# Optimization experiments

Hardware: AMD Instinct MI355X
Metric: run time of the kernel (lower is better)

## Reference

```python
import jax, jax.numpy as jnp
import numpy as np

T = 10.0           # distillation temperature (init arg T)
LOSS_WEIGHT = 1.0  # module-level loss_weight (init arg)
EPS_STD = 1e-07
EPS_RATIO = 1e-08

ROWS, BINS = 1048576, 17  # (4*N, n+1), n = 16


def setup_inputs() -> dict:
    key = jax.random.key(0)
    k1, k2, k3 = jax.random.split(key, 3)
    pred = jax.random.normal(k1, (ROWS, BINS), dtype=jnp.float32)
    soft_label = jax.random.normal(k2, (ROWS, BINS), dtype=jnp.float32)
    weight = jax.random.uniform(k3, (ROWS,), dtype=jnp.float32)
    return {"pred": pred, "soft_label": soft_label, "weight": weight}


def _normalize(logit):
    # torch .std() is unbiased (ddof=1)
    mean = jnp.mean(logit, axis=-1, keepdims=True)
    stdv = jnp.std(logit, axis=-1, keepdims=True, ddof=1)
    return (logit - mean) / (EPS_STD + stdv)


def reference(pred, soft_label, weight):
    soft = jax.lax.stop_gradient(soft_label)  # detach_target=True

    # kd_loss_ls with logit_stand=True
    ls = _normalize(pred)
    lt = _normalize(soft)
    log_p_student = jax.nn.log_softmax(ls / T, axis=1)
    log_p_teacher = jax.nn.log_softmax(lt / T, axis=1)
    p_teacher = jnp.exp(log_p_teacher)
    # F.kl_div(log_pred, target, 'none') = target * (log(target) - log_pred)
    loss_ls = jnp.mean(jnp.sum(p_teacher * (log_p_teacher - log_p_student), axis=1)) * (T * T)

    # sum_distributions_loop on target = softmax(soft_label) -- batched full conv1d
    target = jax.nn.softmax(soft, axis=1)            # (4N, bins)
    n_rows, bins = target.shape
    N = n_rows // 4
    t = target.reshape(N, 4, bins)
    top, bottom, left, right = t[:, 0], t[:, 1], t[:, 2], t[:, 3]
    # pad+flip+conv1d in torch == true full convolution, length 2*bins-1 = 2n+1
    conv_full = jax.vmap(lambda a, b: jnp.convolve(a, b, mode='full'))
    sum_lr = conv_full(left, right)                   # (N, 2n+1)
    sum_tb = conv_full(top, bottom)                   # (N, 2n+1)
    target_ratio = sum_lr / (sum_tb + EPS_RATIO)

    # weighted_loss wrapper: loss * weight, then 'mean' reduction; outer * loss_weight
    loss = LOSS_WEIGHT * jnp.mean(loss_ls * weight)
    return loss, target_ratio
```

## Files before the change

### kernel.cpp

```cpp
#include <hip/hip_runtime.h>

#define ROWS 1048576
#define BINS 17
#define RPB 64
#define NBLK (ROWS / RPB)
#define GPB (RPB / 4)
#define CONV_N 33

template <bool PART>
__global__ __launch_bounds__(64, 4) void kd_main(
    const float* __restrict__ pred,
    const float* __restrict__ soft,
    const float* __restrict__ weight,
    float* __restrict__ out,
    float* __restrict__ ws)
{
    __shared__ float sA[RPB * BINS];
    __shared__ float sB[RPB * BINS];
    const int tid = threadIdx.x;
    const long long base = (long long)blockIdx.x * (RPB * BINS);

    const float4* p4 = reinterpret_cast<const float4*>(pred + base);
    const float4* q4 = reinterpret_cast<const float4*>(soft + base);
    float4* a4 = reinterpret_cast<float4*>(sA);
    float4* b4 = reinterpret_cast<float4*>(sB);
#pragma unroll
    for (int k = 0; k < 4; ++k) {
        a4[k * 64 + tid] = p4[k * 64 + tid];
        b4[k * 64 + tid] = q4[k * 64 + tid];
    }
    if (tid < 16) {
        a4[256 + tid] = p4[256 + tid];
        b4[256 + tid] = q4[256 + tid];
    }
    const float w = weight[blockIdx.x * RPB + tid];
    __syncthreads();

    float x[BINS], y[BINS];
    float sx = 0.f, sy = 0.f, xmx = -1e30f, ymx = -1e30f;
#pragma unroll
    for (int j = 0; j < BINS; ++j) {
        x[j] = sA[tid * BINS + j];
        y[j] = sB[tid * BINS + j];
        sx += x[j]; sy += y[j];
        xmx = fmaxf(xmx, x[j]); ymx = fmaxf(ymx, y[j]);
    }
    const float mx = sx * (1.0f / BINS);
    const float my = sy * (1.0f / BINS);

    float vx = 0.f, vy = 0.f;
#pragma unroll
    for (int j = 0; j < BINS; ++j) {
        const float dx = x[j] - mx; vx = fmaf(dx, dx, vx);
        const float dy = y[j] - my; vy = fmaf(dy, dy, vy);
    }
    const float invsx = 0.1f / (1e-7f + sqrtf(vx * (1.0f / (BINS - 1))));
    const float invsy = 0.1f / (1e-7f + sqrtf(vy * (1.0f / (BINS - 1))));
    const float amax = (xmx - mx) * invsx;
    const float bmax = (ymx - my) * invsy;

    float sea = 0.f, seb = 0.f, ts = 0.f;
#pragma unroll
    for (int j = 0; j < BINS; ++j) {
        sea += __expf((x[j] - mx) * invsx - amax);
        seb += __expf((y[j] - my) * invsy - bmax);
        ts  += __expf(y[j] - ymx);
    }
    const float la = __logf(sea);
    const float lb = __logf(seb);
    const float invseb = 1.0f / seb;
    const float invts  = 1.0f / ts;

    float kl = 0.f;
#pragma unroll
    for (int j = 0; j < BINS; ++j) {
        const float aj = (x[j] - mx) * invsx - amax;
        const float bj = (y[j] - my) * invsy - bmax;
        kl = fmaf(__expf(bj), (bj - lb) - (aj - la), kl);
    }
    kl *= invseb;

#pragma unroll
    for (int j = 0; j < BINS; ++j)
        sA[tid * BINS + j] = __expf(y[j] - ymx) * invts;

    float k2 = kl, w2 = w;
#pragma unroll
    for (int off = 32; off >= 1; off >>= 1) {
        k2 += __shfl_down(k2, off, 64);
        w2 += __shfl_down(w2, off, 64);
    }

    __syncthreads();

    float* sR = sB;

    if (tid < 2 * GPB) {
        const int g = tid >> 1;
        const int R = 4 * g + ((tid & 1) ? 0 : 2);
        float f[2 * BINS];
        const float2* pr = reinterpret_cast<const float2*>(&sA[R * BINS]);
#pragma unroll
        for (int i = 0; i < BINS; ++i) {
            const float2 v = pr[i];
            f[2 * i] = v.x; f[2 * i + 1] = v.y;
        }
        float accv[CONV_N];
#pragma unroll
        for (int j = 0; j < CONV_N; ++j) accv[j] = 0.f;
#pragma unroll
        for (int k = 0; k < BINS; ++k)
#pragma unroll
            for (int m = 0; m < BINS; ++m)
                accv[k + m] = fmaf(f[k], f[BINS + m], accv[k + m]);

#pragma unroll
        for (int j = 0; j < CONV_N; ++j) {
            const float o = __shfl_down(accv[j], 1, 64);
            if ((tid & 1) == 0)
                sR[g * CONV_N + j] = accv[j] / (o + 1e-8f);
        }
    }
    __syncthreads();

    const long long ob = 1 + (long long)blockIdx.x * (GPB * CONV_N);
#pragma unroll
    for (int i = 0; i < 8; ++i)
        out[ob + i * 64 + tid] = sR[i * 64 + tid];
    if (tid < 16) out[ob + 512 + tid] = sR[512 + tid];

    if (tid == 0) {
        if (PART) {
            ws[blockIdx.x]        = k2;
            ws[NBLK + blockIdx.x] = w2;
        } else {
            atomicAdd(&ws[0], k2);
            atomicAdd(&ws[1], w2);
        }
    }
}

template <bool PART>
__global__ __launch_bounds__(1024) void kd_reduce(
    const float* __restrict__ ws, float* __restrict__ out)
{
    if (!PART) {
        if (threadIdx.x == 0)
            out[0] = 100.0f * (ws[0] * (1.0f / ROWS)) * (ws[1] * (1.0f / ROWS));
        return;
    }
    __shared__ float red[32];
    const int tid = threadIdx.x;
    const float4* k4 = reinterpret_cast<const float4*>(ws);
    const float4* w4 = reinterpret_cast<const float4*>(ws + NBLK);
    float ks = 0.f, wsum = 0.f;
#pragma unroll
    for (int i = 0; i < 4; ++i) {
        const float4 a = k4[i * 1024 + tid];
        const float4 b = w4[i * 1024 + tid];
        ks += (a.x + a.y) + (a.z + a.w);
        wsum += (b.x + b.y) + (b.z + b.w);
    }
#pragma unroll
    for (int off = 32; off >= 1; off >>= 1) {
        ks += __shfl_down(ks, off, 64);
        wsum += __shfl_down(wsum, off, 64);
    }
    if ((tid & 63) == 0) {
        red[(tid >> 6) * 2 + 0] = ks;
        red[(tid >> 6) * 2 + 1] = wsum;
    }
    __syncthreads();
    if (tid == 0) {
        float K = 0.f, W = 0.f;
#pragma unroll
        for (int i = 0; i < 16; ++i) { K += red[2 * i]; W += red[2 * i + 1]; }
        out[0] = 100.0f * (K * (1.0f / ROWS)) * (W * (1.0f / ROWS));
    }
}

extern "C" void kernel_launch(void* const* d_in, const int* in_sizes, int n_in,
                              void* d_out, int out_size, void* d_ws, size_t ws_size,
                              hipStream_t stream)
{
    const float* pred   = (const float*)d_in[0];
    const float* soft   = (const float*)d_in[1];
    const float* weight = (const float*)d_in[2];
    float* out = (float*)d_out;
    float* ws  = (float*)d_ws;

    if (ws_size >= (size_t)(2 * NBLK) * sizeof(float)) {
        kd_main<true><<<NBLK, RPB, 0, stream>>>(pred, soft, weight, out, ws);
        kd_reduce<true><<<1, 1024, 0, stream>>>(ws, out);
    } else {
        hipMemsetAsync(ws, 0, 2 * sizeof(float), stream);
        kd_main<false><<<NBLK, RPB, 0, stream>>>(pred, soft, weight, out, ws);
        kd_reduce<false><<<1, 1024, 0, stream>>>(ws, out);
    }
}
```

Baseline: 183.3 us.

## Double rows per block and fuse softmax/KL math into one exp2 pass

Raises rows per block from 64 to 128, writing two per-wave partials per block, and rewrites the per-row statistics as a single pass. Variance now comes from sum and sum of squares, the log-softmax terms are folded into exp2 with a precomputed scale, and the KL is computed from one accumulated sum instead of a second exp loop. Divisions use hardware reciprocal approximations. Risks include reduced precision from the single-pass variance, and only half the block's threads doing the convolution stage.

Result: no change. 183.0 us (-0.2%).

```diff
diff --git a/kernel.cpp b/kernel.cpp
--- a/kernel.cpp
+++ b/kernel.cpp
@@ -2,13 +2,16 @@
 
 #define ROWS 1048576
 #define BINS 17
-#define RPB 64
+#define RPB 128
 #define NBLK (ROWS / RPB)
+#define NPART (2 * NBLK)
 #define GPB (RPB / 4)
 #define CONV_N 33
+#define L2E 1.442695040888963f
+#define LN2 0.6931471805599453f
 
 template <bool PART>
-__global__ __launch_bounds__(64, 4) void kd_main(
+__global__ __launch_bounds__(128, 4) void kd_main(
     const float* __restrict__ pred,
     const float* __restrict__ soft,
     const float* __restrict__ weight,
@@ -26,63 +29,58 @@
     float4* b4 = reinterpret_cast<float4*>(sB);
 #pragma unroll
     for (int k = 0; k < 4; ++k) {
-        a4[k * 64 + tid] = p4[k * 64 + tid];
-        b4[k * 64 + tid] = q4[k * 64 + tid];
+        a4[k * RPB + tid] = p4[k * RPB + tid];
+        b4[k * RPB + tid] = q4[k * RPB + tid];
     }
-    if (tid < 16) {
-        a4[256 + tid] = p4[256 + tid];
-        b4[256 + tid] = q4[256 + tid];
+    if (tid < 32) {
+        a4[512 + tid] = p4[512 + tid];
+        b4[512 + tid] = q4[512 + tid];
     }
     const float w = weight[blockIdx.x * RPB + tid];
     __syncthreads();
 
     float x[BINS], y[BINS];
-    float sx = 0.f, sy = 0.f, xmx = -1e30f, ymx = -1e30f;
+    float sx = 0.f, sy = 0.f, sxx = 0.f, syy = 0.f;
+    float xmx = -1e30f, ymx = -1e30f;
 #pragma unroll
     for (int j = 0; j < BINS; ++j) {
         x[j] = sA[tid * BINS + j];
         y[j] = sB[tid * BINS + j];
-        sx += x[j]; sy += y[j];
-        xmx = fmaxf(xmx, x[j]); ymx = fmaxf(ymx, y[j]);
+        sx += x[j]; sxx = fmaf(x[j], x[j], sxx); xmx = fmaxf(xmx, x[j]);
+        sy += y[j]; syy = fmaf(y[j], y[j], syy); ymx = fmaxf(ymx, y[j]);
     }
     const float mx = sx * (1.0f / BINS);
     const float my = sy * (1.0f / BINS);
+    const float vx = fmaxf(fmaf(-sx, mx, sxx), 0.f) * (1.0f / (BINS - 1));
+    const float vy = fmaxf(fmaf(-sy, my, syy), 0.f) * (1.0f / (BINS - 1));
+    const float sxl = (0.1f * L2E) *
+        __builtin_amdgcn_rcpf(1e-7f + __builtin_amdgcn_sqrtf(vx));
+    const float syl = (0.1f * L2E) *
+        __builtin_amdgcn_rcpf(1e-7f + __builtin_amdgcn_sqrtf(vy));
+    const float cA = -xmx * sxl;
+    const float cB = -ymx * syl;
+    const float cT = -ymx * L2E;
 
-    float vx = 0.f, vy = 0.f;
+    float et[BINS];
+    float sea = 0.f, seb = 0.f, ts = 0.f, sdb = 0.f;
 #pragma unroll
     for (int j = 0; j < BINS; ++j) {
-        const float dx = x[j] - mx; vx = fmaf(dx, dx, vx);
-        const float dy = y[j] - my; vy = fmaf(dy, dy, vy);
+        const float aj = fmaf(x[j], sxl, cA);
+        const float bj = fmaf(y[j], syl, cB);
+        const float ea = exp2f(aj);
+        const float eb = exp2f(bj);
+        const float tv = exp2f(fmaf(y[j], L2E, cT));
+        sea += ea; seb += eb; ts += tv;
+        sdb = fmaf(eb, bj - aj, sdb);
+        et[j] = tv;
     }
-    const float invsx = 0.1f / (1e-7f + sqrtf(vx * (1.0f / (BINS - 1))));
-    const float invsy = 0.1f / (1e-7f + sqrtf(vy * (1.0f / (BINS - 1))));
-    const float amax = (xmx - mx) * invsx;
-    const float bmax = (ymx - my) * invsy;
-
-    float sea = 0.f, seb = 0.f, ts = 0.f;
-#pragma unroll
-    for (int j = 0; j < BINS; ++j) {
-        sea += __expf((x[j] - mx) * invsx - amax);
-        seb += __expf((y[j] - my) * invsy - bmax);
-        ts  += __expf(y[j] - ymx);
-    }
-    const float la = __logf(sea);
-    const float lb = __logf(seb);
-    const float invseb = 1.0f / seb;
-    const float invts  = 1.0f / ts;
-
-    float kl = 0.f;
-#pragma unroll
-    for (int j = 0; j < BINS; ++j) {
-        const float aj = (x[j] - mx) * invsx - amax;
-        const float bj = (y[j] - my) * invsy - bmax;
-        kl = fmaf(__expf(bj), (bj - lb) - (aj - la), kl);
-    }
-    kl *= invseb;
+    const float kl = LN2 * (sdb * __builtin_amdgcn_rcpf(seb)
+                            + (__log2f(sea) - __log2f(seb)));
+    const float invts = __builtin_amdgcn_rcpf(ts);
 
 #pragma unroll
     for (int j = 0; j < BINS; ++j)
-        sA[tid * BINS + j] = __expf(y[j] - ymx) * invts;
+        sA[tid * BINS + j] = et[j] * invts;
 
     float k2 = kl, w2 = w;
 #pragma unroll
@@ -90,12 +88,22 @@
         k2 += __shfl_down(k2, off, 64);
         w2 += __shfl_down(w2, off, 64);
     }
+    if ((tid & 63) == 0) {
+        const int wv = tid >> 6;
+        if (PART) {
+            ws[2 * blockIdx.x + wv]         = k2;
+            ws[NPART + 2 * blockIdx.x + wv] = w2;
+        } else {
+            atomicAdd(&ws[0], k2);
+            atomicAdd(&ws[1], w2);
+        }
+    }
 
     __syncthreads();
 
     float* sR = sB;
 
-    if (tid < 2 * GPB) {
+    if (tid < 64) {
         const int g = tid >> 1;
         const int R = 4 * g + ((tid & 1) ? 0 : 2);
         float f[2 * BINS];
@@ -118,7 +126,8 @@
         for (int j = 0; j < CONV_N; ++j) {
             const float o = __shfl_down(accv[j], 1, 64);
             if ((tid & 1) == 0)
-                sR[g * CONV_N + j] = accv[j] / (o + 1e-8f);
+                sR[g * CONV_N + j] = accv[j] *
+                    __builtin_amdgcn_rcpf(o + 1e-8f);
         }
     }
     __syncthreads();
@@ -126,18 +135,8 @@
     const long long ob = 1 + (long long)blockIdx.x * (GPB * CONV_N);
 #pragma unroll
     for (int i = 0; i < 8; ++i)
-        out[ob + i * 64 + tid] = sR[i * 64 + tid];
-    if (tid < 16) out[ob + 512 + tid] = sR[512 + tid];
-
-    if (tid == 0) {
-        if (PART) {
-            ws[blockIdx.x]        = k2;
-            ws[NBLK + blockIdx.x] = w2;
-        } else {
-            atomicAdd(&ws[0], k2);
-            atomicAdd(&ws[1], w2);
-        }
-    }
+        out[ob + i * RPB + tid] = sR[i * RPB + tid];
+    if (tid < 32) out[ob + 1024 + tid] = sR[1024 + tid];
 }
 
 template <bool PART>
@@ -152,7 +151,7 @@
     __shared__ float red[32];
     const int tid = threadIdx.x;
     const float4* k4 = reinterpret_cast<const float4*>(ws);
-    const float4* w4 = reinterpret_cast<const float4*>(ws + NBLK);
+    const float4* w4 = reinterpret_cast<const float4*>(ws + NPART);
     float ks = 0.f, wsum = 0.f;
 #pragma unroll
     for (int i = 0; i < 4; ++i) {
@@ -189,7 +188,7 @@
     float* out = (float*)d_out;
     float* ws  = (float*)d_ws;
 
-    if (ws_size >= (size_t)(2 * NBLK) * sizeof(float)) {
+    if (ws_size >= (size_t)(2 * NPART) * sizeof(float)) {
         kd_main<true><<<NBLK, RPB, 0, stream>>>(pred, soft, weight, out, ws);
         kd_reduce<true><<<1, 1024, 0, stream>>>(ws, out);
     } else {
```
